# Performance work log

Measured on AMD Instinct MI355X. Metric: run time of the kernel, lower is better.

Reference implementation:

```python
import jax, jax.numpy as jnp
import numpy as np

B, C, T = 8, 64, 2048


def setup_inputs() -> dict:
    key = jax.random.key(0)
    eeg_data = jax.random.normal(key, (B, C, T), dtype=jnp.float32)
    return {"eeg_data": eeg_data}


def _hilbert(signal):
    # FFT-based analytic signal, faithful to the torch code:
    # zero frequencies >= n//2 (even n) or >= (n+1)//2 (odd n), then multiply ALL by 2.
    n = signal.shape[-1]
    spec = jnp.fft.fft(signal, axis=-1)
    cut = n // 2 if n % 2 == 0 else (n + 1) // 2
    keep = (jnp.arange(n) < cut).astype(spec.dtype)
    spec = spec * keep * 2
    return jnp.fft.ifft(spec, axis=-1)


def reference(eeg_data):
    b, c, t = eeg_data.shape
    analytic = _hilbert(eeg_data)
    phase = jnp.angle(analytic)                      # [B, C, T]
    # pairwise phase differences: [B, C, C, T]
    phase_diff = phase[:, :, None, :] - phase[:, None, :, :]
    sin_pd = jnp.sin(phase_diff)
    numerator = jnp.abs(jnp.mean(sin_pd, axis=-1))   # [B, C, C]
    denominator = jnp.mean(jnp.abs(sin_pd), axis=-1)
    denominator = jnp.where(denominator == 0, jnp.float32(1e-8), denominator)
    wpli = numerator / denominator
    eye_mask = 1.0 - jnp.eye(c, dtype=wpli.dtype)[None, :, :]
    return wpli * eye_mask
```

## Files before the change

kernel.cpp:

```cpp
#include <hip/hip_runtime.h>
#include <math.h>

#define T_LEN 2048
#define C_CH  64
#define B_N   8
#define NCHUNK 64

#define IX(a) ((a) + ((a) >> 4))

__device__ __forceinline__ float2 cadd(float2 a, float2 b) { return make_float2(a.x + b.x, a.y + b.y); }
__device__ __forceinline__ float2 csub(float2 a, float2 b) { return make_float2(a.x - b.x, a.y - b.y); }
__device__ __forceinline__ float2 cmul(float2 a, float2 w) {
  return make_float2(a.x * w.x - a.y * w.y, a.x * w.y + a.y * w.x);
}

template <int SIGN>
__device__ __forceinline__ void radix4_stages(float2*& src, float2*& dst,
                                              int tid, const float2* tw) {
  for (int n = 512, ls = 2; n >= 8; n >>= 2, ls += 2) {
    const int s = 1 << ls;
    const int base = (T_LEN - n) / 3;
    for (int idx = tid; idx < 512; idx += 256) {
      const int p = idx >> ls;
      const int q = idx & (s - 1);
      const float2 a = src[IX(idx)];
      const float2 b = src[IX(idx + 512)];
      const float2 c = src[IX(idx + 1024)];
      const float2 d = src[IX(idx + 1536)];
      const float2 t0 = cadd(a, c);
      const float2 t1 = csub(a, c);
      const float2 t2 = cadd(b, d);
      const float2 t3 = csub(b, d);
      const float2 y0 = cadd(t0, t2);
      const float2 r2 = csub(t0, t2);
      float2 r1, r3;
      if (SIGN < 0) {
        r1 = make_float2(t1.x + t3.y, t1.y - t3.x);
        r3 = make_float2(t1.x - t3.y, t1.y + t3.x);
      } else {
        r1 = make_float2(t1.x - t3.y, t1.y + t3.x);
        r3 = make_float2(t1.x + t3.y, t1.y - t3.x);
      }
      float2 w1 = tw[base + p];
      if (SIGN > 0) w1.y = -w1.y;
      const float2 w2 = make_float2(w1.x * w1.x - w1.y * w1.y, 2.0f * w1.x * w1.y);
      const float2 w3 = cmul(w2, w1);
      const int ob = q + 4 * s * p;
      dst[IX(ob)]         = y0;
      dst[IX(ob + s)]     = cmul(r1, w1);
      dst[IX(ob + 2 * s)] = cmul(r2, w2);
      dst[IX(ob + 3 * s)] = cmul(r3, w3);
    }
    __syncthreads();
    float2* tmp = src; src = dst; dst = tmp;
  }
}

__global__ __launch_bounds__(256) void hilbert_phasor_kernel(
    const float* __restrict__ x, float2* __restrict__ phasor) {
  __shared__ float2 bufA[IX(T_LEN - 1) + 1];
  __shared__ float2 bufB[IX(T_LEN - 1) + 1];
  __shared__ float2 tw[682];

  const int bc = blockIdx.x;
  const int tid = threadIdx.x;
  const float* sig = x + (size_t)bc * T_LEN;

  for (int idx = tid; idx < 682; idx += 256) {
    int n, p;
    if (idx < 512)      { n = 2048; p = idx; }
    else if (idx < 640) { n = 512;  p = idx - 512; }
    else if (idx < 672) { n = 128;  p = idx - 640; }
    else if (idx < 680) { n = 32;   p = idx - 672; }
    else                { n = 8;    p = idx - 680; }
    float sn, cs;
    sincosf(-6.28318530717958647692f * (float)p / (float)n, &sn, &cs);
    tw[idx] = make_float2(cs, sn);
  }

  float2* src = bufA;
  float2* dst = bufB;

  for (int idx = tid; idx < 512; idx += 256) {
    const float a = sig[idx];
    const float b = sig[idx + 512];
    const float c = sig[idx + 1024];
    const float d = sig[idx + 1536];
    const float t0 = a + c, t1 = a - c, t2 = b + d, t3 = b - d;
    const float2 w1 = tw[idx];
    const float2 w2 = make_float2(w1.x * w1.x - w1.y * w1.y, 2.0f * w1.x * w1.y);
    const float2 w3 = cmul(w2, w1);
    const float2 r1 = make_float2(t1, -t3);
    const float2 r3 = make_float2(t1,  t3);
    src[IX(4 * idx)]     = make_float2(t0 + t2, 0.0f);
    src[IX(4 * idx + 1)] = cmul(r1, w1);
    src[IX(4 * idx + 2)] = make_float2((t0 - t2) * w2.x, (t0 - t2) * w2.y);
    src[IX(4 * idx + 3)] = cmul(r3, w3);
  }
  __syncthreads();

  radix4_stages<-1>(src, dst, tid, tw);

  for (int q = tid; q < 1024; q += 256) {
    const float2 a = src[IX(q)];
    const float2 b = src[IX(q + 1024)];
    dst[IX(q)]        = cadd(a, b);
    dst[IX(q + 1024)] = csub(a, b);
  }
  __syncthreads();
  { float2* tmp = src; src = dst; dst = tmp; }

  for (int idx = tid; idx < 512; idx += 256) {
    const float2 a = src[IX(idx)];
    const float2 b = src[IX(idx + 512)];
    float2 w1 = tw[idx]; w1.y = -w1.y;
    const float2 w2 = make_float2(w1.x * w1.x - w1.y * w1.y, 2.0f * w1.x * w1.y);
    const float2 w3 = cmul(w2, w1);
    const float2 y0 = cadd(a, b);
    const float2 r2 = csub(a, b);
    const float2 r1 = make_float2(a.x - b.y, a.y + b.x);
    const float2 r3 = make_float2(a.x + b.y, a.y - b.x);
    dst[IX(4 * idx)]     = y0;
    dst[IX(4 * idx + 1)] = cmul(r1, w1);
    dst[IX(4 * idx + 2)] = cmul(r2, w2);
    dst[IX(4 * idx + 3)] = cmul(r3, w3);
  }
  __syncthreads();
  { float2* tmp = src; src = dst; dst = tmp; }

  radix4_stages<1>(src, dst, tid, tw);

  for (int q = tid; q < 1024; q += 256) {
    const float2 a = src[IX(q)];
    const float2 b = src[IX(q + 1024)];
    const float2 zs = cadd(a, b);
    const float2 zd = csub(a, b);
    float2 outv[2] = {zs, zd};
    int    outq[2] = {q, q + 1024};
#pragma unroll
    for (int k = 0; k < 2; ++k) {
      const float2 z = outv[k];
      const float mag2 = z.x * z.x + z.y * z.y;
      float u, v;
      if (mag2 > 0.0f) {
        const float inv = rsqrtf(mag2);
        u = z.x * inv;
        v = z.y * inv;
      } else {
        u = 1.0f;
        v = 0.0f;
      }
      phasor[(size_t)bc * T_LEN + outq[k]] = make_float2(u, v);
    }
  }
}

__global__ __launch_bounds__(256) void wpli_partial_kernel(
    const float2* __restrict__ phasor, float2* __restrict__ part, int nchunk) {
  __shared__ float2 lz[32][65];

  const int c = blockIdx.x;
  const int b = blockIdx.y;
  const int tid = threadIdx.x;
  const int tx = tid & 15;
  const int ty = tid >> 4;

  float accn[4][4] = {{0}}, accd[4][4] = {{0}};

  for (int sub = c; sub < T_LEN / 32; sub += nchunk) {
    const int t0 = sub * 32;
    __syncthreads();
    for (int idx = tid; idx < 2048; idx += 256) {
      const int ch = idx >> 5;
      const int tt = idx & 31;
      lz[tt][ch] = phasor[((size_t)(b * C_CH + ch)) * T_LEN + t0 + tt];
    }
    __syncthreads();

    for (int tt = 0; tt < 32; ++tt) {
      float2 zi[4], zj[4];
#pragma unroll
      for (int a = 0; a < 4; ++a) {
        zi[a] = lz[tt][ty * 4 + a];
        zj[a] = lz[tt][tx * 4 + a];
      }
#pragma unroll
      for (int a = 0; a < 4; ++a)
#pragma unroll
        for (int e = 0; e < 4; ++e) {
          const float s = zi[a].y * zj[e].x - zi[a].x * zj[e].y;
          accn[a][e] += s;
          accd[a][e] += fabsf(s);
        }
    }
  }

  float2* dstp = part + ((size_t)c * B_N + b) * (C_CH * C_CH);
#pragma unroll
  for (int a = 0; a < 4; ++a)
#pragma unroll
    for (int e = 0; e < 4; ++e) {
      const int i = ty * 4 + a;
      const int j = tx * 4 + e;
      dstp[i * C_CH + j] = make_float2(accn[a][e], accd[a][e]);
    }
}

__global__ __launch_bounds__(256) void wpli_finalize_kernel(
    const float2* __restrict__ part, float* __restrict__ out, int nchunk) {
  const int idx = blockIdx.x * 256 + threadIdx.x;
  if (idx >= B_N * C_CH * C_CH) return;
  const int b = idx >> 12;
  const int pair = idx & 4095;
  float n = 0.0f, d = 0.0f;
  for (int c = 0; c < nchunk; ++c) {
    const float2 p = part[((size_t)c * B_N + b) * (C_CH * C_CH) + pair];
    n += p.x;
    d += p.y;
  }
  const int i = pair >> 6;
  const int j = pair & 63;
  float w = (d > 0.0f) ? fabsf(n) / d : 0.0f;
  if (i == j) w = 0.0f;
  out[idx] = w;
}

extern "C" void kernel_launch(void* const* d_in, const int* in_sizes, int n_in,
                              void* d_out, int out_size, void* d_ws, size_t ws_size,
                              hipStream_t stream) {
  const float* eeg = (const float*)d_in[0];
  float* out = (float*)d_out;

  const size_t phasor_bytes = (size_t)B_N * C_CH * T_LEN * sizeof(float2);
  float2* phasor = (float2*)d_ws;
  float2* part = (float2*)((char*)d_ws + phasor_bytes);

  const size_t per_chunk = (size_t)B_N * C_CH * C_CH * sizeof(float2);
  const size_t avail = (ws_size > phasor_bytes) ? ws_size - phasor_bytes : 0;
  int nchunk = NCHUNK;
  while (nchunk > 1 && (size_t)nchunk * per_chunk > avail) nchunk >>= 1;

  hilbert_phasor_kernel<<<B_N * C_CH, 256, 0, stream>>>(eeg, phasor);

  dim3 grid(nchunk, B_N);
  wpli_partial_kernel<<<grid, 256, 0, stream>>>(phasor, part, nchunk);

  wpli_finalize_kernel<<<(B_N * C_CH * C_CH + 255) / 256, 256, 0, stream>>>(
      part, out, nchunk);
}
```

Baseline: 99.85 us.

## Exploit pair antisymmetry to compute only half of channel pairs in wPLI

Uses the antisymmetry of sin(phase_i - phase_j) so each unordered channel pair is accumulated once. A circulant layout assigns each row 32 offsets, and each thread reuses a sliding window of 5 column phasors. The finalize kernel maps each (i,j) back to its stored slot. This halves the inner multiply-accumulate work and the partial-sum traffic, at the cost of modular indexing and duplicated work on the g=32 offset.

```diff
diff --git a/kernel.cpp b/kernel.cpp
--- a/kernel.cpp
+++ b/kernel.cpp
@@ -165,7 +165,7 @@
   const int tx = tid & 15;
   const int ty = tid >> 4;
 
-  float accn[4][4] = {{0}}, accd[4][4] = {{0}};
+  float accn[4][2] = {{0}}, accd[4][2] = {{0}};
 
   for (int sub = c; sub < T_LEN / 32; sub += nchunk) {
     const int t0 = sub * 32;
@@ -177,32 +177,33 @@
     }
     __syncthreads();
 
+    const int jbase = ty * 4 + tx * 2 + 1;
     for (int tt = 0; tt < 32; ++tt) {
-      float2 zi[4], zj[4];
-#pragma unroll
-      for (int a = 0; a < 4; ++a) {
-        zi[a] = lz[tt][ty * 4 + a];
-        zj[a] = lz[tt][tx * 4 + a];
-      }
+      float2 zi[4], zw[5];
+#pragma unroll
+      for (int a = 0; a < 4; ++a) zi[a] = lz[tt][ty * 4 + a];
+#pragma unroll
+      for (int k = 0; k < 5; ++k) zw[k] = lz[tt][(jbase + k) & 63];
 #pragma unroll
       for (int a = 0; a < 4; ++a)
 #pragma unroll
-        for (int e = 0; e < 4; ++e) {
-          const float s = zi[a].y * zj[e].x - zi[a].x * zj[e].y;
+        for (int e = 0; e < 2; ++e) {
+          const float2 zj = zw[a + e];
+          const float s = zi[a].y * zj.x - zi[a].x * zj.y;
           accn[a][e] += s;
           accd[a][e] += fabsf(s);
         }
     }
   }
 
-  float2* dstp = part + ((size_t)c * B_N + b) * (C_CH * C_CH);
+  float2* dstp = part + ((size_t)c * B_N + b) * 2048;
 #pragma unroll
   for (int a = 0; a < 4; ++a)
 #pragma unroll
-    for (int e = 0; e < 4; ++e) {
-      const int i = ty * 4 + a;
-      const int j = tx * 4 + e;
-      dstp[i * C_CH + j] = make_float2(accn[a][e], accd[a][e]);
+    for (int e = 0; e < 2; ++e) {
+      const int r  = ty * 4 + a;
+      const int cc = tx * 2 + e;
+      dstp[r * 32 + cc] = make_float2(accn[a][e], accd[a][e]);
     }
 }
 
@@ -212,16 +213,23 @@
   if (idx >= B_N * C_CH * C_CH) return;
   const int b = idx >> 12;
   const int pair = idx & 4095;
-  float n = 0.0f, d = 0.0f;
-  for (int c = 0; c < nchunk; ++c) {
-    const float2 p = part[((size_t)c * B_N + b) * (C_CH * C_CH) + pair];
-    n += p.x;
-    d += p.y;
-  }
   const int i = pair >> 6;
   const int j = pair & 63;
-  float w = (d > 0.0f) ? fabsf(n) / d : 0.0f;
-  if (i == j) w = 0.0f;
+  const int g = (j - i) & 63;
+  float w = 0.0f;
+  if (g != 0) {
+    int r, cc;
+    if (g <= 32) { r = i; cc = g - 1; }
+    else         { r = j; cc = 63 - g; }
+    const int slot = r * 32 + cc;
+    float n = 0.0f, d = 0.0f;
+    for (int c = 0; c < nchunk; ++c) {
+      const float2 p = part[((size_t)c * B_N + b) * 2048 + slot];
+      n += p.x;
+      d += p.y;
+    }
+    w = (d > 0.0f) ? fabsf(n) / d : 0.0f;
+  }
   out[idx] = w;
 }
 
@@ -235,7 +243,7 @@
   float2* phasor = (float2*)d_ws;
   float2* part = (float2*)((char*)d_ws + phasor_bytes);
 
-  const size_t per_chunk = (size_t)B_N * C_CH * C_CH * sizeof(float2);
+  const size_t per_chunk = (size_t)B_N * 2048 * sizeof(float2);
   const size_t avail = (ws_size > phasor_bytes) ? ws_size - phasor_bytes : 0;
   int nchunk = NCHUNK;
   while (nchunk > 1 && (size_t)nchunk * per_chunk > avail) nchunk >>= 1;
```

Measured after the change: 97.76 us. 2.1% less time.
